# Performance work log

Measured on AMD Instinct MI355X. Metric: run time of the kernel, lower is better.

## Reference

```python
import jax, jax.numpy as jnp
import numpy as np

C = 128      # in channels
CO = 64      # out channels
G = 32       # group-norm groups
RES_IN = 32  # input resolution
RES_OUT = 64 # subdivided resolution
N = 20000    # active input voxels
EPS = 1e-5


def setup_inputs() -> dict:
    key = jax.random.key(0)
    ks = jax.random.split(key, 12)
    # unique active voxel coords at RES_IN (batch index 0, single instance)
    rng = np.random.default_rng(0)
    flat = rng.choice(RES_IN ** 3, size=N, replace=False)
    xyz = np.stack([flat // (RES_IN * RES_IN), (flat // RES_IN) % RES_IN, flat % RES_IN], axis=1)
    x_coords = jnp.asarray(np.concatenate([np.zeros((N, 1), np.int32), xyz.astype(np.int32)], axis=1))
    x_feats = jax.random.normal(ks[0], (N, C), dtype=jnp.float32)
    gn1_g = 1.0 + 0.1 * jax.random.normal(ks[1], (C,), dtype=jnp.float32)
    gn1_b = 0.1 * jax.random.normal(ks[2], (C,), dtype=jnp.float32)
    W1 = 0.05 * jax.random.normal(ks[3], (3, 3, 3, C, CO), dtype=jnp.float32)
    b1 = 0.01 * jax.random.normal(ks[4], (CO,), dtype=jnp.float32)
    gn2_g = 1.0 + 0.1 * jax.random.normal(ks[5], (CO,), dtype=jnp.float32)
    gn2_b = 0.1 * jax.random.normal(ks[6], (CO,), dtype=jnp.float32)
    W2 = 0.05 * jax.random.normal(ks[7], (3, 3, 3, CO, CO), dtype=jnp.float32)  # zero_module in source; random here to exercise math
    b2 = 0.01 * jax.random.normal(ks[8], (CO,), dtype=jnp.float32)
    Ws = 0.05 * jax.random.normal(ks[9], (C, CO), dtype=jnp.float32)   # 1x1 skip conv
    bs = 0.01 * jax.random.normal(ks[10], (CO,), dtype=jnp.float32)
    return dict(x_feats=x_feats, x_coords=x_coords, gn1_g=gn1_g, gn1_b=gn1_b,
                W1=W1, b1=b1, gn2_g=gn2_g, gn2_b=gn2_b, W2=W2, b2=b2, Ws=Ws, bs=bs)


def group_norm(f, g, b):
    # single-instance sparse group norm: stats per group over all points
    n, c = f.shape
    x = f.reshape(n, G, c // G)
    mu = jnp.mean(x, axis=(0, 2), keepdims=True)
    var = jnp.mean((x - mu) ** 2, axis=(0, 2), keepdims=True)
    return ((x - mu) * jax.lax.rsqrt(var + EPS)).reshape(n, c) * g + b


def subdivide(coords, feats):
    n = coords.shape[0]
    offs = jnp.stack(jnp.meshgrid(jnp.arange(2), jnp.arange(2), jnp.arange(2), indexing='ij'), -1).reshape(8, 3)
    xyz = coords[:, None, 1:] * 2 + offs[None].astype(coords.dtype)          # [n,8,3]
    bidx = jnp.broadcast_to(coords[:, None, :1], (n, 8, 1))
    new_coords = jnp.concatenate([bidx, xyz], axis=-1).reshape(n * 8, 4)
    return new_coords, jnp.repeat(feats, 8, axis=0)


def subm_conv3(coords, feats, W, b):
    # submanifold 3x3x3 sparse conv: scatter to padded dense grid, gather 27 neighbors per active site
    cin = feats.shape[1]
    grid = jnp.zeros((RES_OUT + 2, RES_OUT + 2, RES_OUT + 2, cin), feats.dtype)
    grid = grid.at[coords[:, 1] + 1, coords[:, 2] + 1, coords[:, 3] + 1].set(feats)
    acc = jnp.zeros((feats.shape[0], W.shape[-1]), feats.dtype)
    for i in range(3):
        for j in range(3):
            for k in range(3):
                nb = grid[coords[:, 1] + i, coords[:, 2] + j, coords[:, 3] + k]  # [n, cin]
                acc = acc + nb @ W[i, j, k]
    return acc + b


def reference(x_feats, x_coords, gn1_g, gn1_b, W1, b1, gn2_g, gn2_b, W2, b2, Ws, bs):
    h = jax.nn.silu(group_norm(x_feats, gn1_g, gn1_b))
    hc, hf = subdivide(x_coords, h)
    _, xf = subdivide(x_coords, x_feats)
    hf = subm_conv3(hc, hf, W1, b1)
    hf = jax.nn.silu(group_norm(hf, gn2_g, gn2_b))
    hf = subm_conv3(hc, hf, W2, b2)
    out = hf + (xf @ Ws + bs)  # residual + 1x1 skip conv (out_channels != channels)
    return out
```

## Files before the change

### kernel.cpp

```cpp
#include <hip/hip_runtime.h>
#include <hip/hip_bf16.h>
#include <math.h>

#define N_PTS 20000
#define C_IN 128
#define C_OUT 64
#define M_PTS (N_PTS*8)
#define EPS 1e-5f

typedef __attribute__((ext_vector_type(8))) short short8;
typedef __attribute__((ext_vector_type(4))) float float4v;

__device__ __forceinline__ ushort f2bf(float f){
    unsigned int i = __float_as_uint(f);
    unsigned int r = i + 0x7fffu + ((i >> 16) & 1u);
    return (ushort)(r >> 16);
}
__device__ __forceinline__ float bf2f(ushort u){ return __uint_as_float(((unsigned int)u) << 16); }
__device__ __forceinline__ float silu(float z){ return z / (1.f + expf(-z)); }


__global__ void __launch_bounds__(256) prep_kernel(
    const float* __restrict__ W1, const float* __restrict__ W2,
    ushort* __restrict__ Wt1, ushort* __restrict__ Wt2,
    int* __restrict__ pg, ushort* __restrict__ h, ushort* __restrict__ h2,
    const float* __restrict__ x, float* __restrict__ stats)
{
    const int b = blockIdx.x, tid = threadIdx.x;
    if (b < 2048){
        int idx = b * 256 + tid;
        int j = idx & 7, l = (idx >> 3) & 63, nb = (idx >> 9) & 3, kb = (idx >> 11) & 3, t = idx >> 13;
        int ci = kb * 32 + (l >> 4) * 8 + j, co = nb * 16 + (l & 15);
        int o = t >> 3, jj = t & 7;
        int ox = (o >> 2) & 1, oy = (o >> 1) & 1, oz = o & 1;
        int jx = (jj >> 2) & 1, jy = (jj >> 1) & 1, jz = jj & 1;
        float s = 0.f;
#pragma unroll
        for (int dx = -1; dx <= 1; dx++){
            if (((ox + dx) >> 1) != ox + jx - 1) continue;
#pragma unroll
            for (int dy = -1; dy <= 1; dy++){
                if (((oy + dy) >> 1) != oy + jy - 1) continue;
#pragma unroll
                for (int dz = -1; dz <= 1; dz++){
                    if (((oz + dz) >> 1) != oz + jz - 1) continue;
                    s += W1[((dx+1)*9 + (dy+1)*3 + (dz+1)) * (C_IN*64) + ci * 64 + co];
                }
            }
        }
        Wt1[idx] = f2bf(s);
    } else if (b < 2480){
        int idx = (b - 2048) * 256 + tid;
        int j = idx & 7, l = (idx >> 3) & 63, nb = (idx >> 9) & 3, kb = (idx >> 11) & 1, t = idx >> 12;
        int ci = kb * 32 + (l >> 4) * 8 + j, co = nb * 16 + (l & 15);
        Wt2[idx] = f2bf(W2[(t * C_OUT + ci) * 64 + co]);
    } else if (b < 2608){
        int i = (b - 2480) * 256 + tid;
        pg[i] = -1;
        if (b == 2480){
            if (tid < C_IN) h[(size_t)N_PTS * C_IN + tid] = 0;
            if (tid < 256){
                h2[(size_t)M_PTS * C_OUT + tid] = 0;
                h2[(size_t)M_PTS * C_OUT + 256 + tid] = 0;
            }
        }
    } else {
        __shared__ float ls[64];
        if (tid < 64) ls[tid] = 0.f;
        __syncthreads();
        const int g = tid & 31;
        const int r0 = (b - 2608) * 8 + (tid >> 5);
        float sum = 0.f, sq = 0.f;
        for (int r = r0; r < N_PTS; r += 4096){
            float4 v = *(const float4*)(x + (size_t)r * C_IN + g * 4);
            sum += v.x + v.y + v.z + v.w;
            sq  += v.x*v.x + v.y*v.y + v.z*v.z + v.w*v.w;
        }
        atomicAdd(&ls[g], sum);
        atomicAdd(&ls[32 + g], sq);
        __syncthreads();
        if (tid < 64) atomicAdd(&stats[tid], ls[tid]);
    }
}

__global__ void __launch_bounds__(256) mid_kernel(
    const int* __restrict__ cds, int* __restrict__ pg,
    const float* __restrict__ x, const float* __restrict__ stats,
    const float* __restrict__ g1, const float* __restrict__ b1, ushort* __restrict__ h,
    const float* __restrict__ Wsk, const float* __restrict__ bsk, float* __restrict__ s)
{
    __shared__ float w[C_IN * C_OUT];
    const int b = blockIdx.x, tid = threadIdx.x;
    if (b < 79){
        int i = b * 256 + tid;
        if (i < N_PTS){
            const int* cd = cds + i * 4;
            pg[(cd[1] * 32 + cd[2]) * 32 + cd[3]] = i;
        }
    } else if (b < 2579){
        int i = ((b - 79) * 256 + tid) * 4;
        int c0 = i & (C_IN - 1);
        int g = c0 >> 2;
        float mu = stats[g] * (1.0f / (N_PTS * 4.0f));
        float var = stats[32 + g] * (1.0f / (N_PTS * 4.0f)) - mu * mu;
        float rs = rsqrtf(var + EPS);
        float4 v = *(const float4*)(x + i);
        ushort4 o;
        o.x = f2bf(silu((v.x - mu) * rs * g1[c0+0] + b1[c0+0]));
        o.y = f2bf(silu((v.y - mu) * rs * g1[c0+1] + b1[c0+1]));
        o.z = f2bf(silu((v.z - mu) * rs * g1[c0+2] + b1[c0+2]));
        o.w = f2bf(silu((v.w - mu) * rs * g1[c0+3] + b1[c0+3]));
        *(ushort4*)(h + i) = o;
    } else {
        for (int j = tid; j < C_IN * C_OUT; j += 256) w[j] = Wsk[j];
        __syncthreads();
        int co = tid & 63, pr = tid >> 6;
        int p = (b - 2579) * 4 + pr;
        const float* xr = x + (size_t)p * C_IN;
        float a = bsk[co];
        for (int cb = 0; cb < C_IN; cb += 4){
            float4 v = *(const float4*)(xr + cb);
            a += v.x * w[(cb+0)*64+co] + v.y * w[(cb+1)*64+co]
               + v.z * w[(cb+2)*64+co] + v.w * w[(cb+3)*64+co];
        }
        s[(size_t)p * C_OUT + co] = a;
    }
}

__global__ void __launch_bounds__(256, 2) conv1_corner(
    const ushort* __restrict__ feat, const int* __restrict__ pg,
    const int* __restrict__ coords, const ushort* __restrict__ Wt,
    const float* __restrict__ bias, ushort* __restrict__ hf1_bf,
    float* __restrict__ statsAcc)
{
    const int tid = threadIdx.x;
    const int wid = tid >> 6, l = tid & 63;
    const int r16 = l & 15, qd = l >> 4;
    const int b = blockIdx.x;
    const int tg = (b >> 6) * 8 + (b & 7);
    const int o  = (b >> 3) & 7;
    if (tg >= 79) return;
    const int tile = tg * 4 + wid;
    if (tile >= 313) return;
    const int mb = tile * 64;

    int p = mb + l;
    int pc = p < N_PTS ? p : N_PTS - 1;
    int px = coords[pc*4+1], py = coords[pc*4+2], pz = coords[pc*4+3];
    int ex0 = px + ((o >> 2) & 1) - 1;
    int ey0 = py + ((o >> 1) & 1) - 1;
    int ez0 = pz + (o & 1) - 1;

    int rows8[8];
#pragma unroll
    for (int j = 0; j < 8; j++){
        int cx = ex0 + ((j >> 2) & 1), cy = ey0 + ((j >> 1) & 1), cz = ez0 + (j & 1);
        int row = N_PTS;
        if ((unsigned)cx < 32u && (unsigned)cy < 32u && (unsigned)cz < 32u){
            int pi = pg[cx * 1024 + cy * 32 + cz];
            if (pi >= 0) row = pi;
        }
        rows8[j] = row;
    }

    float4v acc[16];
#pragma unroll
    for (int c = 0; c < 16; c++) acc[c] = 0.f;

#pragma unroll
    for (int j = 0; j < 8; j++){
        int fr0 = __shfl(rows8[j],      r16, 64);
        int fr1 = __shfl(rows8[j], 16 + r16, 64);
        int fr2 = __shfl(rows8[j], 32 + r16, 64);
        int fr3 = __shfl(rows8[j], 48 + r16, 64);
        const ushort* a0 = feat + (size_t)fr0 * C_IN + qd * 8;
        const ushort* a1 = feat + (size_t)fr1 * C_IN + qd * 8;
        const ushort* a2 = feat + (size_t)fr2 * C_IN + qd * 8;
        const ushort* a3 = feat + (size_t)fr3 * C_IN + qd * 8;
        const ushort* wt = Wt + (size_t)(o * 8 + j) * 8192 + l * 8;
#pragma unroll
        for (int kb = 0; kb < 4; kb++){
            short8 b0 = *(const short8*)(wt + (kb*4+0)*512);
            short8 b1 = *(const short8*)(wt + (kb*4+1)*512);
            short8 b2 = *(const short8*)(wt + (kb*4+2)*512);
            short8 b3 = *(const short8*)(wt + (kb*4+3)*512);
            short8 av0 = *(const short8*)(a0 + kb*32);
            short8 av1 = *(const short8*)(a1 + kb*32);
            short8 av2 = *(const short8*)(a2 + kb*32);
            short8 av3 = *(const short8*)(a3 + kb*32);
            acc[0]  = __builtin_amdgcn_mfma_f32_16x16x32_bf16(av0, b0, acc[0],  0, 0, 0);
            acc[1]  = __builtin_amdgcn_mfma_f32_16x16x32_bf16(av0, b1, acc[1],  0, 0, 0);
            acc[2]  = __builtin_amdgcn_mfma_f32_16x16x32_bf16(av0, b2, acc[2],  0, 0, 0);
            acc[3]  = __builtin_amdgcn_mfma_f32_16x16x32_bf16(av0, b3, acc[3],  0, 0, 0);
            acc[4]  = __builtin_amdgcn_mfma_f32_16x16x32_bf16(av1, b0, acc[4],  0, 0, 0);
            acc[5]  = __builtin_amdgcn_mfma_f32_16x16x32_bf16(av1, b1, acc[5],  0, 0, 0);
            acc[6]  = __builtin_amdgcn_mfma_f32_16x16x32_bf16(av1, b2, acc[6],  0, 0, 0);
            acc[7]  = __builtin_amdgcn_mfma_f32_16x16x32_bf16(av1, b3, acc[7],  0, 0, 0);
            acc[8]  = __builtin_amdgcn_mfma_f32_16x16x32_bf16(av2, b0, acc[8],  0, 0, 0);
            acc[9]  = __builtin_amdgcn_mfma_f32_16x16x32_bf16(av2, b1, acc[9],  0, 0, 0);
            acc[10] = __builtin_amdgcn_mfma_f32_16x16x32_bf16(av2, b2, acc[10], 0, 0, 0);
            acc[11] = __builtin_amdgcn_mfma_f32_16x16x32_bf16(av2, b3, acc[11], 0, 0, 0);
            acc[12] = __builtin_amdgcn_mfma_f32_16x16x32_bf16(av3, b0, acc[12], 0, 0, 0);
            acc[13] = __builtin_amdgcn_mfma_f32_16x16x32_bf16(av3, b1, acc[13], 0, 0, 0);
            acc[14] = __builtin_amdgcn_mfma_f32_16x16x32_bf16(av3, b2, acc[14], 0, 0, 0);
            acc[15] = __builtin_amdgcn_mfma_f32_16x16x32_bf16(av3, b3, acc[15], 0, 0, 0);
        }
    }

    float bsv[4] = { bias[r16], bias[16 + r16], bias[32 + r16], bias[48 + r16] };
    float ps[4] = {0,0,0,0}, pq[4] = {0,0,0,0};
#pragma unroll
    for (int rb = 0; rb < 4; rb++)
#pragma unroll
        for (int nb = 0; nb < 4; nb++)
#pragma unroll
            for (int rg = 0; rg < 4; rg++){
                int pr = mb + rb * 16 + qd * 4 + rg;
                float v = acc[rb * 4 + nb][rg] + bsv[nb];
                if (pr < N_PTS){
                    hf1_bf[(size_t)(pr * 8 + o) * 64 + nb * 16 + r16] = f2bf(v);
                    ps[nb] += v; pq[nb] += v * v;
                }
            }
#pragma unroll
    for (int nb = 0; nb < 4; nb++){
        float s1 = ps[nb], s2 = pq[nb];
        s1 += __shfl_xor(s1, 16, 64); s2 += __shfl_xor(s2, 16, 64);
        s1 += __shfl_xor(s1, 32, 64); s2 += __shfl_xor(s2, 32, 64);
        if (qd == 0){
            atomicAdd(&statsAcc[64 + nb * 16 + r16], s1);
            atomicAdd(&statsAcc[128 + nb * 16 + r16], s2);
        }
    }
}

__global__ void __launch_bounds__(512, 2) conv2_corner(
    const ushort* __restrict__ feat, const int* __restrict__ pg,
    const int* __restrict__ coords, const ushort* __restrict__ Wt,
    const float* __restrict__ bias, const float* __restrict__ skip,
    float* __restrict__ out)
{
    const int tid = threadIdx.x;
    const int o = tid >> 6, l = tid & 63;
    const int r16 = l & 15, qd = l >> 4;
    const int bx = blockIdx.x;
    const int ox = (o >> 2) & 1, oy = (o >> 1) & 1, oz = o & 1;
    const int mb = bx * 64;

    int p = mb + l;
    int pc = p < N_PTS ? p : N_PTS - 1;
    int px = coords[pc*4+1], py = coords[pc*4+2], pz = coords[pc*4+3];
    int ex0 = px + ox - 1, ey0 = py + oy - 1, ez0 = pz + oz - 1;

    int pb[8];
#pragma unroll
    for (int j = 0; j < 8; j++){
        int cx = ex0 + ((j >> 2) & 1), cy = ey0 + ((j >> 1) & 1), cz = ez0 + (j & 1);
        int base = M_PTS;
        if ((unsigned)cx < 32u && (unsigned)cy < 32u && (unsigned)cz < 32u){
            int pi = pg[cx * 1024 + cy * 32 + cz];
            if (pi >= 0) base = pi * 8;
        }
        pb[j] = base;
    }

    float4v acc[16];
#pragma unroll
    for (int c = 0; c < 16; c++) acc[c] = 0.f;

#pragma unroll
    for (int t = 0; t < 27; t++){
        const int dx = t / 9 - 1, dy = (t / 3) % 3 - 1, dz = t % 3 - 1;
        int sx = ox + dx, sy = oy + dy, sz = oz + dz;
        int jx = (sx >> 1) - ox + 1, jy = (sy >> 1) - oy + 1, jz = (sz >> 1) - oz + 1;
        int opi = (sx & 1) * 4 + (sy & 1) * 2 + (sz & 1);
        int m00 = jz ? pb[1] : pb[0];
        int m01 = jz ? pb[3] : pb[2];
        int m10 = jz ? pb[5] : pb[4];
        int m11 = jz ? pb[7] : pb[6];
        int n0 = jy ? m01 : m00;
        int n1 = jy ? m11 : m10;
        int row = (jx ? n1 : n0) + opi;
        int fr0 = __shfl(row,      r16, 64);
        int fr1 = __shfl(row, 16 + r16, 64);
        int fr2 = __shfl(row, 32 + r16, 64);
        int fr3 = __shfl(row, 48 + r16, 64);
        const ushort* a0 = feat + (size_t)fr0 * C_OUT + qd * 8;
        const ushort* a1 = feat + (size_t)fr1 * C_OUT + qd * 8;
        const ushort* a2 = feat + (size_t)fr2 * C_OUT + qd * 8;
        const ushort* a3 = feat + (size_t)fr3 * C_OUT + qd * 8;
        const ushort* wt = Wt + (size_t)t * 4096 + l * 8;
#pragma unroll
        for (int kb = 0; kb < 2; kb++){
            short8 b0 = *(const short8*)(wt + (kb*4+0)*512);
            short8 b1 = *(const short8*)(wt + (kb*4+1)*512);
            short8 b2 = *(const short8*)(wt + (kb*4+2)*512);
            short8 b3 = *(const short8*)(wt + (kb*4+3)*512);
            short8 av0 = *(const short8*)(a0 + kb*32);
            short8 av1 = *(const short8*)(a1 + kb*32);
            short8 av2 = *(const short8*)(a2 + kb*32);
            short8 av3 = *(const short8*)(a3 + kb*32);
            acc[0]  = __builtin_amdgcn_mfma_f32_16x16x32_bf16(av0, b0, acc[0],  0, 0, 0);
            acc[1]  = __builtin_amdgcn_mfma_f32_16x16x32_bf16(av0, b1, acc[1],  0, 0, 0);
            acc[2]  = __builtin_amdgcn_mfma_f32_16x16x32_bf16(av0, b2, acc[2],  0, 0, 0);
            acc[3]  = __builtin_amdgcn_mfma_f32_16x16x32_bf16(av0, b3, acc[3],  0, 0, 0);
            acc[4]  = __builtin_amdgcn_mfma_f32_16x16x32_bf16(av1, b0, acc[4],  0, 0, 0);
            acc[5]  = __builtin_amdgcn_mfma_f32_16x16x32_bf16(av1, b1, acc[5],  0, 0, 0);
            acc[6]  = __builtin_amdgcn_mfma_f32_16x16x32_bf16(av1, b2, acc[6],  0, 0, 0);
            acc[7]  = __builtin_amdgcn_mfma_f32_16x16x32_bf16(av1, b3, acc[7],  0, 0, 0);
            acc[8]  = __builtin_amdgcn_mfma_f32_16x16x32_bf16(av2, b0, acc[8],  0, 0, 0);
            acc[9]  = __builtin_amdgcn_mfma_f32_16x16x32_bf16(av2, b1, acc[9],  0, 0, 0);
            acc[10] = __builtin_amdgcn_mfma_f32_16x16x32_bf16(av2, b2, acc[10], 0, 0, 0);
            acc[11] = __builtin_amdgcn_mfma_f32_16x16x32_bf16(av2, b3, acc[11], 0, 0, 0);
            acc[12] = __builtin_amdgcn_mfma_f32_16x16x32_bf16(av3, b0, acc[12], 0, 0, 0);
            acc[13] = __builtin_amdgcn_mfma_f32_16x16x32_bf16(av3, b1, acc[13], 0, 0, 0);
            acc[14] = __builtin_amdgcn_mfma_f32_16x16x32_bf16(av3, b2, acc[14], 0, 0, 0);
            acc[15] = __builtin_amdgcn_mfma_f32_16x16x32_bf16(av3, b3, acc[15], 0, 0, 0);
        }
    }

    float bsv[4] = { bias[r16], bias[16 + r16], bias[32 + r16], bias[48 + r16] };
#pragma unroll
    for (int rb = 0; rb < 4; rb++)
#pragma unroll
        for (int rg = 0; rg < 4; rg++){
            int pr = mb + rb * 16 + qd * 4 + rg;
            if (pr < N_PTS){
                const float* sk = skip + (size_t)pr * 64;
#pragma unroll
                for (int nb = 0; nb < 4; nb++){
                    int co = nb * 16 + r16;
                    out[(size_t)(pr * 8 + o) * 64 + co] = acc[rb * 4 + nb][rg] + bsv[nb] + sk[co];
                }
            }
        }
}

__global__ void __launch_bounds__(256) h2_kernel(
    const ushort* __restrict__ hf1, const float* __restrict__ stats,
    const float* __restrict__ gg, const float* __restrict__ gb, ushort* __restrict__ h2)
{
    int i = (blockIdx.x * 256 + threadIdx.x) * 4;
    if (i >= M_PTS * C_OUT) return;
    int c0 = i & (C_OUT - 1);
    const float inv = 1.0f / (M_PTS * 2.0f);
    float muA = (stats[64 + c0] + stats[64 + c0 + 1]) * inv;
    float vA  = (stats[128 + c0] + stats[128 + c0 + 1]) * inv - muA * muA;
    float rsA = rsqrtf(vA + EPS);
    float muB = (stats[64 + c0 + 2] + stats[64 + c0 + 3]) * inv;
    float vB  = (stats[128 + c0 + 2] + stats[128 + c0 + 3]) * inv - muB * muB;
    float rsB = rsqrtf(vB + EPS);
    ushort4 u = *(const ushort4*)(hf1 + i);
    ushort4 o;
    o.x = f2bf(silu((bf2f(u.x) - muA) * rsA * gg[c0+0] + gb[c0+0]));
    o.y = f2bf(silu((bf2f(u.y) - muA) * rsA * gg[c0+1] + gb[c0+1]));
    o.z = f2bf(silu((bf2f(u.z) - muB) * rsB * gg[c0+2] + gb[c0+2]));
    o.w = f2bf(silu((bf2f(u.w) - muB) * rsB * gg[c0+3] + gb[c0+3]));
    *(ushort4*)(h2 + i) = o;
}

extern "C" void kernel_launch(void* const* d_in, const int* in_sizes, int n_in,
                              void* d_out, int out_size, void* d_ws, size_t ws_size,
                              hipStream_t stream){
    const float* x   = (const float*)d_in[0];
    const int*   cds = (const int*)  d_in[1];
    const float* g1  = (const float*)d_in[2];
    const float* b1  = (const float*)d_in[3];
    const float* W1  = (const float*)d_in[4];
    const float* bb1 = (const float*)d_in[5];
    const float* g2  = (const float*)d_in[6];
    const float* b2  = (const float*)d_in[7];
    const float* W2  = (const float*)d_in[8];
    const float* bb2 = (const float*)d_in[9];
    const float* Wsk = (const float*)d_in[10];
    const float* bsk = (const float*)d_in[11];
    float* out = (float*)d_out;
    char* ws = (char*)d_ws;

    float*  stats = (float*) (ws);
    int*    pg    = (int*)   (ws + 1024);
    ushort* h     = (ushort*)(ws + 132096);
    ushort* h2    = (ushort*)(ws + 5252352);
    float*  s     = (float*) (ws + 25733376);
    ushort* Wt1   = (ushort*)(ws + 30853376);
    ushort* Wt2   = (ushort*)(ws + 31901952);

    hipMemsetAsync(stats, 0, 192 * sizeof(float), stream);
    prep_kernel<<<3120, 256, 0, stream>>>(W1, W2, Wt1, Wt2, pg, h, h2, x, stats);
    mid_kernel<<<7579, 256, 0, stream>>>(cds, pg, x, stats, g1, b1, h, Wsk, bsk, s);
    conv1_corner<<<640, 256, 0, stream>>>(h, pg, cds, Wt1, bb1, (ushort*)d_out, stats);
    h2_kernel<<<12500, 256, 0, stream>>>((const ushort*)d_out, stats, g2, b2, h2);
    conv2_corner<<<313, 512, 0, stream>>>(h2, pg, cds, Wt2, bb2, s, out);
}
```

Baseline: 378.0 us.

## Reorder active voxels along a Morton curve to improve neighbor gather locality

Adds a single-block sort kernel that walks the 32^3 grid in Morton order, assigns each active voxel a rank, and rewrites the position grid to store ranks. Features, skip outputs and intermediate activations are then laid out in Morton order, so the 27-neighbor gathers in both convolutions hit nearby rows and cache better. The final conv scatters results back to the original point order using the packed original index. Also splits conv2 into 256-thread blocks with two corner halves per tile and raises the occupancy hints. The cost is an extra serial one-block kernel and indirect writes.

Result: slower. 402.0 us (+6.3%).

```diff
diff --git a/kernel.cpp b/kernel.cpp
--- a/kernel.cpp
+++ b/kernel.cpp
@@ -18,6 +18,10 @@
 }
 __device__ __forceinline__ float bf2f(ushort u){ return __uint_as_float(((unsigned int)u) << 16); }
 __device__ __forceinline__ float silu(float z){ return z / (1.f + expf(-z)); }
+__device__ __forceinline__ int cmp5(int v){
+    v &= 0x1249; v = (v | (v >> 2)) & 0x10C3; v = (v | (v >> 4)) & 0x100F; v = (v | (v >> 8)) & 0x1F;
+    return v;
+}
 
 
 __global__ void __launch_bounds__(256) prep_kernel(
@@ -83,23 +87,62 @@
     }
 }
 
+__global__ void __launch_bounds__(256) scatter_kernel(
+    const int* __restrict__ cds, int* __restrict__ pg)
+{
+    int i = blockIdx.x * 256 + threadIdx.x;
+    if (i < N_PTS){
+        const int* cd = cds + i * 4;
+        pg[(cd[1] * 32 + cd[2]) * 32 + cd[3]] = i;
+    }
+}
+
+__global__ void __launch_bounds__(1024) sort_kernel(
+    int* __restrict__ pg, unsigned int* __restrict__ ordp)
+{
+    __shared__ int psum[1024];
+    const int t = threadIdx.x;
+    int cnt = 0;
+    for (int i = 0; i < 32; i++){
+        int m = t * 32 + i;
+        int x = cmp5(m >> 2), y = cmp5(m >> 1), z = cmp5(m);
+        cnt += (pg[(x * 32 + y) * 32 + z] >= 0) ? 1 : 0;
+    }
+    psum[t] = cnt;
+    __syncthreads();
+    for (int off = 1; off < 1024; off <<= 1){
+        int v = (t >= off) ? psum[t - off] : 0;
+        __syncthreads();
+        psum[t] += v;
+        __syncthreads();
+    }
+    int run = psum[t] - cnt;
+    for (int i = 0; i < 32; i++){
+        int m = t * 32 + i;
+        int x = cmp5(m >> 2), y = cmp5(m >> 1), z = cmp5(m);
+        int ci = (x * 32 + y) * 32 + z;
+        int pi = pg[ci];
+        if (pi >= 0){
+            ordp[run] = ((unsigned int)pi << 15) | (unsigned int)((x << 10) | (y << 5) | z);
+            pg[ci] = run;
+            run++;
+        }
+    }
+}
+
 __global__ void __launch_bounds__(256) mid_kernel(
-    const int* __restrict__ cds, int* __restrict__ pg,
+    const int* __restrict__ cds, const int* __restrict__ pg,
     const float* __restrict__ x, const float* __restrict__ stats,
     const float* __restrict__ g1, const float* __restrict__ b1, ushort* __restrict__ h,
     const float* __restrict__ Wsk, const float* __restrict__ bsk, float* __restrict__ s)
 {
     __shared__ float w[C_IN * C_OUT];
     const int b = blockIdx.x, tid = threadIdx.x;
-    if (b < 79){
-        int i = b * 256 + tid;
-        if (i < N_PTS){
-            const int* cd = cds + i * 4;
-            pg[(cd[1] * 32 + cd[2]) * 32 + cd[3]] = i;
-        }
-    } else if (b < 2579){
-        int i = ((b - 79) * 256 + tid) * 4;
-        int c0 = i & (C_IN - 1);
+    if (b < 2500){
+        int i = (b * 256 + tid) * 4;
+        int row = i >> 7, c0 = i & 127;
+        const int* cd = cds + row * 4;
+        int rk = pg[(cd[1] * 32 + cd[2]) * 32 + cd[3]];
         int g = c0 >> 2;
         float mu = stats[g] * (1.0f / (N_PTS * 4.0f));
         float var = stats[32 + g] * (1.0f / (N_PTS * 4.0f)) - mu * mu;
@@ -110,12 +153,14 @@
         o.y = f2bf(silu((v.y - mu) * rs * g1[c0+1] + b1[c0+1]));
         o.z = f2bf(silu((v.z - mu) * rs * g1[c0+2] + b1[c0+2]));
         o.w = f2bf(silu((v.w - mu) * rs * g1[c0+3] + b1[c0+3]));
-        *(ushort4*)(h + i) = o;
+        *(ushort4*)(h + (size_t)rk * C_IN + c0) = o;
     } else {
         for (int j = tid; j < C_IN * C_OUT; j += 256) w[j] = Wsk[j];
         __syncthreads();
         int co = tid & 63, pr = tid >> 6;
-        int p = (b - 2579) * 4 + pr;
+        int p = (b - 2500) * 4 + pr;
+        const int* cd = cds + p * 4;
+        int rk = pg[(cd[1] * 32 + cd[2]) * 32 + cd[3]];
         const float* xr = x + (size_t)p * C_IN;
         float a = bsk[co];
         for (int cb = 0; cb < C_IN; cb += 4){
@@ -123,13 +168,13 @@
             a += v.x * w[(cb+0)*64+co] + v.y * w[(cb+1)*64+co]
                + v.z * w[(cb+2)*64+co] + v.w * w[(cb+3)*64+co];
         }
-        s[(size_t)p * C_OUT + co] = a;
-    }
-}
-
-__global__ void __launch_bounds__(256, 2) conv1_corner(
+        s[(size_t)rk * C_OUT + co] = a;
+    }
+}
+
+__global__ void __launch_bounds__(256, 4) conv1_corner(
     const ushort* __restrict__ feat, const int* __restrict__ pg,
-    const int* __restrict__ coords, const ushort* __restrict__ Wt,
+    const unsigned int* __restrict__ ordp, const ushort* __restrict__ Wt,
     const float* __restrict__ bias, ushort* __restrict__ hf1_bf,
     float* __restrict__ statsAcc)
 {
@@ -144,9 +189,10 @@
     if (tile >= 313) return;
     const int mb = tile * 64;
 
-    int p = mb + l;
-    int pc = p < N_PTS ? p : N_PTS - 1;
-    int px = coords[pc*4+1], py = coords[pc*4+2], pz = coords[pc*4+3];
+    int slot = mb + l;
+    int cs = slot < N_PTS ? slot : N_PTS - 1;
+    int cell = (int)(ordp[cs] & 0x7FFFu);
+    int px = (cell >> 10) & 31, py = (cell >> 5) & 31, pz = cell & 31;
     int ex0 = px + ((o >> 2) & 1) - 1;
     int ey0 = py + ((o >> 1) & 1) - 1;
     int ez0 = pz + (o & 1) - 1;
@@ -215,7 +261,8 @@
         for (int nb = 0; nb < 4; nb++)
 #pragma unroll
             for (int rg = 0; rg < 4; rg++){
-                int pr = mb + rb * 16 + qd * 4 + rg;
+                int sl = rb * 16 + qd * 4 + rg;
+                int pr = mb + sl;
                 float v = acc[rb * 4 + nb][rg] + bsv[nb];
                 if (pr < N_PTS){
                     hf1_bf[(size_t)(pr * 8 + o) * 64 + nb * 16 + r16] = f2bf(v);
@@ -234,22 +281,27 @@
     }
 }
 
-__global__ void __launch_bounds__(512, 2) conv2_corner(
+__global__ void __launch_bounds__(256, 4) conv2_corner(
     const ushort* __restrict__ feat, const int* __restrict__ pg,
-    const int* __restrict__ coords, const ushort* __restrict__ Wt,
-    const float* __restrict__ bias, const float* __restrict__ skip,
-    float* __restrict__ out)
+    const unsigned int* __restrict__ ordp,
+    const ushort* __restrict__ Wt, const float* __restrict__ bias,
+    const float* __restrict__ skip, float* __restrict__ out)
 {
     const int tid = threadIdx.x;
-    const int o = tid >> 6, l = tid & 63;
+    const int wid = tid >> 6, l = tid & 63;
     const int r16 = l & 15, qd = l >> 4;
-    const int bx = blockIdx.x;
+    const int b = blockIdx.x;
+    const int tile = b >> 1;
+    const int o = (b & 1) * 4 + wid;
     const int ox = (o >> 2) & 1, oy = (o >> 1) & 1, oz = o & 1;
-    const int mb = bx * 64;
-
-    int p = mb + l;
-    int pc = p < N_PTS ? p : N_PTS - 1;
-    int px = coords[pc*4+1], py = coords[pc*4+2], pz = coords[pc*4+3];
+    const int mb = tile * 64;
+
+    int slot = mb + l;
+    int cs = slot < N_PTS ? slot : N_PTS - 1;
+    unsigned int op = ordp[cs];
+    int sp = (int)(op >> 15);
+    int cell = (int)(op & 0x7FFFu);
+    int px = (cell >> 10) & 31, py = (cell >> 5) & 31, pz = cell & 31;
     int ex0 = px + ox - 1, ey0 = py + oy - 1, ez0 = pz + oz - 1;
 
     int pb[8];
@@ -324,13 +376,15 @@
     for (int rb = 0; rb < 4; rb++)
 #pragma unroll
         for (int rg = 0; rg < 4; rg++){
-            int pr = mb + rb * 16 + qd * 4 + rg;
-            if (pr < N_PTS){
-                const float* sk = skip + (size_t)pr * 64;
+            int sl = rb * 16 + qd * 4 + rg;
+            int slt = mb + sl;
+            if (slt < N_PTS){
+                int spr = __shfl(sp, sl, 64);
+                const float* sk = skip + (size_t)slt * 64;
 #pragma unroll
                 for (int nb = 0; nb < 4; nb++){
                     int co = nb * 16 + r16;
-                    out[(size_t)(pr * 8 + o) * 64 + co] = acc[rb * 4 + nb][rg] + bsv[nb] + sk[co];
+                    out[(size_t)(spr * 8 + o) * 64 + co] = acc[rb * 4 + nb][rg] + bsv[nb] + sk[co];
                 }
             }
         }
@@ -384,11 +438,14 @@
     float*  s     = (float*) (ws + 25733376);
     ushort* Wt1   = (ushort*)(ws + 30853376);
     ushort* Wt2   = (ushort*)(ws + 31901952);
+    unsigned int* ordp = (unsigned int*)(ws + 32123136);
 
     hipMemsetAsync(stats, 0, 192 * sizeof(float), stream);
     prep_kernel<<<3120, 256, 0, stream>>>(W1, W2, Wt1, Wt2, pg, h, h2, x, stats);
-    mid_kernel<<<7579, 256, 0, stream>>>(cds, pg, x, stats, g1, b1, h, Wsk, bsk, s);
-    conv1_corner<<<640, 256, 0, stream>>>(h, pg, cds, Wt1, bb1, (ushort*)d_out, stats);
+    scatter_kernel<<<79, 256, 0, stream>>>(cds, pg);
+    sort_kernel<<<1, 1024, 0, stream>>>(pg, ordp);
+    mid_kernel<<<7500, 256, 0, stream>>>(cds, pg, x, stats, g1, b1, h, Wsk, bsk, s);
+    conv1_corner<<<640, 256, 0, stream>>>(h, pg, ordp, Wt1, bb1, (ushort*)d_out, stats);
     h2_kernel<<<12500, 256, 0, stream>>>((const ushort*)d_out, stats, g2, b2, h2);
-    conv2_corner<<<313, 512, 0, stream>>>(h2, pg, cds, Wt2, bb2, s, out);
-}
+    conv2_corner<<<626, 256, 0, stream>>>(h2, pg, ordp, Wt2, bb2, s, out);
+}
```
